# Performance work log

Measured on AMD Instinct MI355X. Metric: run time of the kernel, lower is better.

## Reference

```python
import jax, jax.numpy as jnp
import numpy as np

B, L, DM, H = 2, 2048, 512, 8
D = DM // H
FACTOR = 5
NUM_K = int(FACTOR * np.ceil(np.log(L)))  # 40
NUM_Q = NUM_K  # q_len == k_len here
EPS = 1e-5


def setup_inputs() -> dict:
    key = jax.random.key(0)
    ks = jax.random.split(key, 12)
    s = DM ** -0.5
    return {
        "q": jax.random.normal(ks[0], (B, L, DM), jnp.float32),
        "k": jax.random.normal(ks[1], (B, L, DM), jnp.float32),
        "v": jax.random.normal(ks[2], (B, L, DM), jnp.float32),
        "Wq": jax.random.normal(ks[3], (DM, DM), jnp.float32) * s,
        "bq": jnp.zeros((DM,), jnp.float32),
        "Wk": jax.random.normal(ks[4], (DM, DM), jnp.float32) * s,
        "bk": jnp.zeros((DM,), jnp.float32),
        "Wv": jax.random.normal(ks[5], (DM, DM), jnp.float32) * s,
        "bv": jnp.zeros((DM,), jnp.float32),
        "gamma": jnp.ones((DM,), jnp.float32),
        "beta": jnp.zeros((DM,), jnp.float32),
        "random_index": jax.random.randint(ks[6], (L, NUM_K), 0, L, jnp.int32),
    }


def _heads(x):
    # [B, L, DM] -> [B, H, L, D]
    return x.reshape(B, L, H, D).transpose(0, 2, 1, 3)


def reference(q, k, v, Wq, bq, Wk, bk, Wv, bv, gamma, beta, random_index):
    qp = _heads(q @ Wq + bq)
    kp = _heads(k @ Wk + bk)
    vp = _heads(v @ Wv + bv)

    # ProbSparse: sample NUM_K keys per query position (shared over batch/head)
    k_samp = kp[:, :, random_index, :]                      # [B,H,L,NUM_K,D]
    pre = jnp.einsum('bhid,bhijd->bhij', qp, k_samp)        # [B,H,L,NUM_K]
    measure = pre.max(-1) - pre.sum(-1) / L                 # sparsity measure [B,H,L]
    _, q_idx = jax.lax.top_k(measure, NUM_Q)                # [B,H,NUM_Q]

    q_sel = jnp.take_along_axis(qp, q_idx[..., None], axis=2)   # [B,H,NUM_Q,D]
    attn = jnp.einsum('bhid,bhjd->bhij', q_sel, kp) * D ** -0.5 # [B,H,NUM_Q,L]
    attn = jax.nn.softmax(attn, axis=-1)                    # dropout = identity (eval)
    out_sel = jnp.einsum('bhij,bhjd->bhid', attn, vp)       # [B,H,NUM_Q,D]

    # use_mask=False path: context is the mean of v over keys
    v_mean = vp.mean(axis=2)                                # [B,H,D]
    context = jnp.broadcast_to(v_mean[:, :, None, :], (B, H, L, D))
    bi = jnp.arange(B)[:, None, None]
    hi = jnp.arange(H)[None, :, None]
    out = context.at[bi, hi, q_idx].set(out_sel)            # scatter selected rows

    out = out.transpose(0, 2, 1, 3).reshape(B, L, DM)
    y = out + q
    mu = y.mean(-1, keepdims=True)
    var = y.var(-1, keepdims=True)
    yn = (y - mu) / jnp.sqrt(var + EPS) * gamma + beta
    return (yn, attn)
```

## Files before the change

### kernel.cpp

```cpp
#include <hip/hip_runtime.h>
#include <math.h>

#define BB 2
#define LL 2048
#define DMM 512
#define HH 8
#define DD 64
#define NUMK 40
#define NUMQ 40
#define LNEPS 1e-5f
#define LSEG 128
#define NLS 16

typedef unsigned short ushort_t;
typedef __attribute__((ext_vector_type(8))) short bf16x8;
typedef __attribute__((ext_vector_type(4))) float f32x4;

__device__ inline ushort_t f2bf(float x) {
    union { float f; unsigned int u; } v; v.f = x;
    unsigned int r = v.u + 0x7fffu + ((v.u >> 16) & 1u);
    return (ushort_t)(r >> 16);
}
__device__ inline float bf2f(ushort_t h) {
    union { unsigned int u; float f; } v; v.u = ((unsigned int)h) << 16;
    return v.f;
}

__global__ __launch_bounds__(256) void convert_all_kernel(
    const float* __restrict__ q, const float* __restrict__ k, const float* __restrict__ v,
    const float* __restrict__ Wq, const float* __restrict__ Wk, const float* __restrict__ Wv,
    ushort_t* __restrict__ Xh, ushort_t* __restrict__ Xl,
    ushort_t* __restrict__ Wht, ushort_t* __restrict__ Wlt) {
    __shared__ float tile[64][65];
    const int bx = blockIdx.x;
    const int t = threadIdx.x;
    if (bx < 3072) {
        const int y = bx >> 10, x = bx & 1023;
        const size_t plane = (size_t)BB * LL * DMM;
        const float* X = (y == 0) ? q : (y == 1) ? k : v;
        ushort_t* xh = Xh + plane * y;
        ushort_t* xl = Xl + plane * y;
        const size_t base = ((size_t)x * 256 + t) * 8;
        float4 a = *(const float4*)(X + base);
        float4 b = *(const float4*)(X + base + 4);
        float xs[8] = {a.x, a.y, a.z, a.w, b.x, b.y, b.z, b.w};
        unsigned int hp[4], lp[4];
#pragma unroll
        for (int j = 0; j < 4; ++j) {
            ushort_t h0 = f2bf(xs[2 * j]),     h1 = f2bf(xs[2 * j + 1]);
            ushort_t l0 = f2bf(xs[2 * j] - bf2f(h0));
            ushort_t l1 = f2bf(xs[2 * j + 1] - bf2f(h1));
            hp[j] = (unsigned int)h0 | ((unsigned int)h1 << 16);
            lp[j] = (unsigned int)l0 | ((unsigned int)l1 << 16);
        }
        *(uint4*)(xh + base) = make_uint4(hp[0], hp[1], hp[2], hp[3]);
        *(uint4*)(xl + base) = make_uint4(lp[0], lp[1], lp[2], lp[3]);
    } else {
        const int idx = bx - 3072;
        const int z = idx >> 6, rem = idx & 63;
        const size_t plane = (size_t)DMM * DMM;
        const float* W = (z == 0) ? Wq : (z == 1) ? Wk : Wv;
        ushort_t* wht = Wht + plane * z;
        ushort_t* wlt = Wlt + plane * z;
        const int n0 = (rem & 7) * 64, k0 = (rem >> 3) * 64;
        const int d = t & 63, g = t >> 6;
        for (int rr = g; rr < 64; rr += 4)
            tile[rr][d] = W[(size_t)(k0 + rr) * DMM + n0 + d];
        __syncthreads();
        for (int cc = g; cc < 64; cc += 4) {
            float x = tile[d][cc];
            ushort_t hi = f2bf(x);
            ushort_t lo = f2bf(x - bf2f(hi));
            wht[(size_t)(n0 + cc) * DMM + k0 + d] = hi;
            wlt[(size_t)(n0 + cc) * DMM + k0 + d] = lo;
        }
    }
}

__device__ inline void stage_one(const ushort_t* __restrict__ g, ushort_t* lbuf,
                                 int r0, int lane, int k0) {
    const int r = r0 + (lane >> 3);
    const int c = (lane & 7) ^ (r & 7);
    const ushort_t* gp = g + (size_t)r * DMM + k0 + c * 8;
    __builtin_amdgcn_global_load_lds(
        (const __attribute__((address_space(1))) unsigned int*)gp,
        (__attribute__((address_space(3))) unsigned int*)(lbuf + (size_t)r0 * 64),
        16, 0, 0);
}
__device__ inline bf16x8 frag_ld(const ushort_t* buf, int row, int c) {
    const int idx = row * 8 + (c ^ (row & 7));
    return *(const bf16x8*)(buf + idx * 8);
}

__global__ __launch_bounds__(256, 2) void proj_mfma_kernel(
    const ushort_t* __restrict__ Xh, const ushort_t* __restrict__ Xl,
    const ushort_t* __restrict__ Wht, const ushort_t* __restrict__ Wlt,
    const float* __restrict__ bq, const float* __restrict__ bk, const float* __restrict__ bv,
    float* __restrict__ Oq, float* __restrict__ Ok, float* __restrict__ Ov) {
    const int orig = blockIdx.x;
    const int c = (orig & 7) * 48 + (orig >> 3);
    const int jb = c & 3, mb = (c >> 2) & 31, z = c >> 7;

    const size_t xplane = (size_t)BB * LL * DMM;
    const size_t wplane = (size_t)DMM * DMM;
    const ushort_t* ah_g = Xh + xplane * z;
    const ushort_t* al_g = Xl + xplane * z;
    const ushort_t* bh_g = Wht + wplane * z;
    const ushort_t* bl_g = Wlt + wplane * z;
    const float* bias = (z == 0) ? bq : (z == 1) ? bk : bv;
    float* Out = (z == 0) ? Oq : (z == 1) ? Ok : Ov;

    __shared__ __align__(16) ushort_t bufAh[128 * 64];
    __shared__ __align__(16) ushort_t bufAl[128 * 64];
    __shared__ __align__(16) ushort_t bufBh[128 * 64];
    __shared__ __align__(16) ushort_t bufBl[128 * 64];

    const int t = threadIdx.x;
    const int lane = t & 63, w = t >> 6;
    const int wm = (w & 1) * 64, wn = (w >> 1) * 64;
    const int m0 = mb * 128, j0 = jb * 128;

    const ushort_t* A_h = ah_g + (size_t)m0 * DMM;
    const ushort_t* A_l = al_g + (size_t)m0 * DMM;
    const ushort_t* B_h = bh_g + (size_t)j0 * DMM;
    const ushort_t* B_l = bl_g + (size_t)j0 * DMM;

    f32x4 acc[4][4];
#pragma unroll
    for (int i = 0; i < 4; ++i)
#pragma unroll
        for (int j = 0; j < 4; ++j) acc[i][j] = (f32x4){0.f, 0.f, 0.f, 0.f};

    for (int ch = 0; ch < 8; ++ch) {
        const int k0 = ch * 64;
#pragma unroll
        for (int i = 0; i < 4; ++i) {
            const int r0 = (w * 4 + i) * 8;
            stage_one(A_h, bufAh, r0, lane, k0);
            stage_one(A_l, bufAl, r0, lane, k0);
            stage_one(B_h, bufBh, r0, lane, k0);
            stage_one(B_l, bufBl, r0, lane, k0);
        }
        __syncthreads();
#pragma unroll
        for (int ks = 0; ks < 2; ++ks) {
            const int cc = ks * 4 + (lane >> 4);
            bf16x8 fah[4], fal[4];
#pragma unroll
            for (int tm = 0; tm < 4; ++tm) {
                const int row = wm + tm * 16 + (lane & 15);
                fah[tm] = frag_ld(bufAh, row, cc);
                fal[tm] = frag_ld(bufAl, row, cc);
            }
#pragma unroll
            for (int tn = 0; tn < 4; ++tn) {
                const int rowb = wn + tn * 16 + (lane & 15);
                const bf16x8 fbh = frag_ld(bufBh, rowb, cc);
                const bf16x8 fbl = frag_ld(bufBl, rowb, cc);
#pragma unroll
                for (int tm = 0; tm < 4; ++tm) {
                    acc[tm][tn] = __builtin_amdgcn_mfma_f32_16x16x32_bf16(fah[tm], fbh, acc[tm][tn], 0, 0, 0);
                    acc[tm][tn] = __builtin_amdgcn_mfma_f32_16x16x32_bf16(fal[tm], fbh, acc[tm][tn], 0, 0, 0);
                    acc[tm][tn] = __builtin_amdgcn_mfma_f32_16x16x32_bf16(fah[tm], fbl, acc[tm][tn], 0, 0, 0);
                }
            }
        }
        __syncthreads();
    }

#pragma unroll
    for (int tn = 0; tn < 4; ++tn) {
        const int gn = j0 + wn + tn * 16 + (lane & 15);
        const float bvv = bias[gn];
        const int h = gn >> 6, d = gn & 63;
#pragma unroll
        for (int tm = 0; tm < 4; ++tm) {
#pragma unroll
            for (int reg = 0; reg < 4; ++reg) {
                const int gm = m0 + wm + tm * 16 + (lane >> 4) * 4 + reg;
                const int b = gm >> 11, l = gm & (LL - 1);
                Out[(((size_t)(b * HH + h)) * LL + l) * DD + d] = acc[tm][tn][reg] + bvv;
            }
        }
    }
}

__global__ __launch_bounds__(256) void measure_vmean_kernel(
    const float* __restrict__ qp2, const float* __restrict__ kp2,
    const float* __restrict__ vp2, const int* __restrict__ rnd,
    float* __restrict__ measure, float* __restrict__ partial) {
    __shared__ float pv[256];
    const int bx = blockIdx.x;
    const int t = threadIdx.x;
    if (bx < 2048) {
        const int c = (bx & 7) * 256 + (bx >> 3);
        const int lane = t & 63;
        const int wv = t >> 6;
        const int g = lane >> 4;
        const int dq = (lane & 15) * 4;
        const int bh = c >> 7;
        const int i = (c & 127) * 16 + wv * 4 + g;
        const float4 qv = *(const float4*)(qp2 + ((size_t)bh * LL + i) * DD + dq);
        const float* kbase = kp2 + (size_t)bh * LL * DD;
        const int* rp = rnd + i * NUMK;
        float mx = -INFINITY, sm = 0.f;
#pragma unroll 8
        for (int j = 0; j < NUMK; ++j) {
            const int row = rp[j];
            const float4 kv = *(const float4*)(kbase + (size_t)row * DD + dq);
            float p = kv.x * qv.x;
            p = fmaf(kv.y, qv.y, p); p = fmaf(kv.z, qv.z, p); p = fmaf(kv.w, qv.w, p);
            p += __shfl_xor(p, 1, 64);
            p += __shfl_xor(p, 2, 64);
            p += __shfl_xor(p, 4, 64);
            p += __shfl_xor(p, 8, 64);
            mx = fmaxf(mx, p);
            sm += p;
        }
        if ((lane & 15) == 0) measure[(size_t)bh * LL + i] = mx - sm * (1.0f / LL);
    } else {
        const int idx = bx - 2048;
        const int chunk = idx & 31;
        const int bh = idx >> 5;
        const int d = t & 63, g = t >> 6;
        const int l0 = chunk * 64;
        float acc = 0.f;
        for (int l = l0 + g; l < l0 + 64; l += 4)
            acc += vp2[((size_t)bh * LL + l) * DD + d];
        pv[t] = acc;
        __syncthreads();
        if (t < 64)
            partial[(size_t)idx * 64 + t] = pv[t] + pv[64 + t] + pv[128 + t] + pv[192 + t];
    }
}

__global__ __launch_bounds__(256) void topk_kernel(const float* __restrict__ measure,
                                                   const float* __restrict__ partial,
                                                   int* __restrict__ q_idx,
                                                   int* __restrict__ sel_pos,
                                                   float* __restrict__ v_mean) {
    __shared__ unsigned int keys[LL];
    __shared__ int hist[256];
    __shared__ unsigned int prefix_sh;
    __shared__ int need_sh;
    __shared__ unsigned int cval[256];
    __shared__ int cidx[256];
    __shared__ int cnt;
    const int t = threadIdx.x;
    const int lane = t & 63;
    const int bh = blockIdx.x;
    for (int i = t; i < LL; i += 256) {
        const float f = measure[(size_t)bh * LL + i];
        unsigned int u = __float_as_uint(f);
        keys[i] = (u & 0x80000000u) ? ~u : (u | 0x80000000u);
        sel_pos[(size_t)bh * LL + i] = -1;
    }
    if (t < 64) {
        float s = 0.f;
        for (int c = 0; c < 32; ++c)
            s += partial[((size_t)bh * 32 + c) * 64 + t];
        v_mean[bh * 64 + t] = s * (1.0f / LL);
    }
    if (t == 0) { prefix_sh = 0u; need_sh = NUMQ; cnt = 0; }
    __syncthreads();

    for (int round = 0; round < 4; ++round) {
        const int shift = 24 - round * 8;
        hist[t] = 0;
        __syncthreads();
        const unsigned int pref = prefix_sh;
        if (round == 0) {
            for (int i = t; i < LL; i += 256) {
                const int b = (int)(keys[i] >> 24);
                unsigned long long rem = ~0ull;
                while (rem) {
                    const int leader = __ffsll((long long)rem) - 1;
                    const int b0 = __shfl(b, leader, 64);
                    const unsigned long long same = __ballot(b == b0) & rem;
                    if (lane == leader) atomicAdd(&hist[b0], (int)__popcll(same));
                    rem &= ~same;
                }
            }
        } else {
            const unsigned int mask = 0xFFFFFFFFu << (shift + 8);
            for (int i = t; i < LL; i += 256) {
                const unsigned int key = keys[i];
                if ((key & mask) == pref)
                    atomicAdd(&hist[(key >> shift) & 0xFF], 1);
            }
        }
        __syncthreads();
        if (t < 64) {
            const int b0 = hist[4 * t + 0], b1 = hist[4 * t + 1];
            const int b2 = hist[4 * t + 2], b3 = hist[4 * t + 3];
            const int loc = b0 + b1 + b2 + b3;
            int suf = loc;
#pragma unroll
            for (int off = 1; off < 64; off <<= 1) {
                const int other = __shfl_down(suf, off, 64);
                if (lane + off < 64) suf += other;
            }
            const int need = need_sh;
            int s[5];
            s[0] = suf;
            s[1] = suf - b0;
            s[2] = suf - b0 - b1;
            s[3] = suf - b0 - b1 - b2;
            s[4] = suf - loc;
#pragma unroll
            for (int kk = 0; kk < 4; ++kk) {
                if (s[kk] >= need && s[kk + 1] < need) {
                    need_sh = need - s[kk + 1];
                    prefix_sh = pref | ((unsigned int)(4 * t + kk) << shift);
                }
            }
        }
        __syncthreads();
    }
    const unsigned int K40 = prefix_sh;

    for (int i = t; i < LL; i += 256) {
        if (keys[i] >= K40) {
            int p = atomicAdd(&cnt, 1);
            if (p < 256) { cval[p] = keys[i]; cidx[p] = i; }
        }
    }
    __syncthreads();
    int M = cnt; if (M > 256) M = 256;
    for (int i = t; i < M; i += 256) {
        const unsigned int ki = cval[i];
        const int ii = cidx[i];
        int r = 0;
        for (int j = 0; j < M; ++j) {
            const unsigned int kj = cval[j];
            r += (kj > ki || (kj == ki && cidx[j] < ii)) ? 1 : 0;
        }
        if (r < NUMQ) {
            q_idx[bh * NUMQ + r] = ii;
            sel_pos[(size_t)bh * LL + ii] = r;
        }
    }
}

__global__ __launch_bounds__(256) void attn_part_kernel(
    const float* __restrict__ qp2, const float* __restrict__ kp2,
    const float* __restrict__ vp2, const int* __restrict__ q_idx,
    float* __restrict__ attn_out, float* __restrict__ part_m,
    float* __restrict__ part_s, float* __restrict__ part_pv) {
    __shared__ __align__(16) float Qs[NUMQ][68];
    __shared__ __align__(16) float Ks[LSEG * 64];
    __shared__ __align__(16) float Vs[LSEG * 64];
    __shared__ __align__(16) float Ss[NUMQ][136];
    const int t = threadIdx.x;
    const int lane = t & 63, w = t >> 6;
    const int bh = blockIdx.x;
    const int ls = blockIdx.y;
    const int l0 = ls * LSEG;

    for (int idx = t; idx < NUMQ * 16; idx += 256) {
        const int r = idx >> 4, c4 = idx & 15;
        const int qi = q_idx[bh * NUMQ + r];
        float4 v = *(const float4*)(qp2 + ((size_t)bh * LL + qi) * DD + c4 * 4);
        Qs[r][c4 * 4 + 0] = v.x * 0.125f;
        Qs[r][c4 * 4 + 1] = v.y * 0.125f;
        Qs[r][c4 * 4 + 2] = v.z * 0.125f;
        Qs[r][c4 * 4 + 3] = v.w * 0.125f;
    }

    const float* kseg = kp2 + ((size_t)bh * LL + l0) * DD;
    const float* vseg = vp2 + ((size_t)bh * LL + l0) * DD;
#pragma unroll
    for (int i = 0; i < 8; ++i) {
        const int r0 = (w * 8 + i) * 4;
        const int r = r0 + (lane >> 4);
        const int cg = (lane & 15) ^ (r & 15);
        __builtin_amdgcn_global_load_lds(
            (const __attribute__((address_space(1))) unsigned int*)(kseg + (size_t)r * DD + cg * 4),
            (__attribute__((address_space(3))) unsigned int*)(Ks + r0 * 64), 16, 0, 0);
        __builtin_amdgcn_global_load_lds(
            (const __attribute__((address_space(1))) unsigned int*)(vseg + (size_t)r * DD + cg * 4),
            (__attribute__((address_space(3))) unsigned int*)(Vs + r0 * 64), 16, 0, 0);
    }
    __syncthreads();

    const int qt = t >> 5;
    const int jt = t & 31;
    float acc[5][4];
#pragma unroll
    for (int i = 0; i < 5; ++i)
#pragma unroll
        for (int jj = 0; jj < 4; ++jj) acc[i][jj] = 0.f;

    for (int c4 = 0; c4 < 16; ++c4) {
        float4 q4[5];
#pragma unroll
        for (int i = 0; i < 5; ++i)
            q4[i] = *(const float4*)&Qs[qt + 8 * i][c4 * 4];
#pragma unroll
        for (int jj = 0; jj < 4; ++jj) {
            const int r = jt + 32 * jj;
            const float4 k4 = *(const float4*)&Ks[r * 64 + ((c4 ^ (r & 15)) * 4)];
#pragma unroll
            for (int i = 0; i < 5; ++i) {
                acc[i][jj] = fmaf(q4[i].x, k4.x, acc[i][jj]);
                acc[i][jj] = fmaf(q4[i].y, k4.y, acc[i][jj]);
                acc[i][jj] = fmaf(q4[i].z, k4.z, acc[i][jj]);
                acc[i][jj] = fmaf(q4[i].w, k4.w, acc[i][jj]);
            }
        }
    }

#pragma unroll
    for (int i = 0; i < 5; ++i) {
        const int r = qt + 8 * i;
        float m = fmaxf(fmaxf(acc[i][0], acc[i][1]), fmaxf(acc[i][2], acc[i][3]));
        m = fmaxf(m, __shfl_xor(m, 16, 64));
        m = fmaxf(m, __shfl_xor(m, 8, 64));
        m = fmaxf(m, __shfl_xor(m, 4, 64));
        m = fmaxf(m, __shfl_xor(m, 2, 64));
        m = fmaxf(m, __shfl_xor(m, 1, 64));
        float p0 = __expf(acc[i][0] - m), p1 = __expf(acc[i][1] - m);
        float p2 = __expf(acc[i][2] - m), p3 = __expf(acc[i][3] - m);
        Ss[r][jt]      = p0;
        Ss[r][jt + 32] = p1;
        Ss[r][jt + 64] = p2;
        Ss[r][jt + 96] = p3;
        float s = p0 + p1 + p2 + p3;
        s += __shfl_xor(s, 16, 64);
        s += __shfl_xor(s, 8, 64);
        s += __shfl_xor(s, 4, 64);
        s += __shfl_xor(s, 2, 64);
        s += __shfl_xor(s, 1, 64);
        if (jt == 0) {
            const int row = bh * NUMQ + r;
            part_m[row * NLS + ls] = m;
            part_s[row * NLS + ls] = s;
        }
    }
    __syncthreads();

    for (int idx = t; idx < NUMQ * 32; idx += 256) {
        const int r = idx >> 5, c4 = idx & 31;
        const float4 v = *(const float4*)&Ss[r][c4 * 4];
        *(float4*)(attn_out + (size_t)(bh * NUMQ + r) * LL + l0 + c4 * 4) = v;
    }

    const int dt = t & 31;
    float o[5][2];
#pragma unroll
    for (int i = 0; i < 5; ++i) { o[i][0] = 0.f; o[i][1] = 0.f; }
#pragma unroll 2
    for (int j0_ = 0; j0_ < LSEG; j0_ += 4) {
        float4 p4[5];
#pragma unroll
        for (int i = 0; i < 5; ++i)
            p4[i] = *(const float4*)&Ss[qt + 8 * i][j0_];
#pragma unroll
        for (int jj = 0; jj < 4; ++jj) {
            const int j = j0_ + jj;
            const int pg = (dt >> 1) ^ (j & 15);
            const float* vr = &Vs[j * 64 + pg * 4 + (dt & 1) * 2];
            const float v0 = vr[0], v1 = vr[1];
#pragma unroll
            for (int i = 0; i < 5; ++i) {
                const float p = ((const float*)&p4[i])[jj];
                o[i][0] = fmaf(p, v0, o[i][0]);
                o[i][1] = fmaf(p, v1, o[i][1]);
            }
        }
    }
#pragma unroll
    for (int i = 0; i < 5; ++i) {
        const int row = bh * NUMQ + qt + 8 * i;
        float* pp = part_pv + ((size_t)row * NLS + ls) * DD + dt * 2;
        pp[0] = o[i][0];
        pp[1] = o[i][1];
    }
}

__global__ __launch_bounds__(512) void final_all_kernel(
    const float* __restrict__ q_in, const int* __restrict__ sel_pos,
    const float* __restrict__ part_m, const float* __restrict__ part_s,
    const float* __restrict__ part_pv, const float* __restrict__ v_mean,
    const float* __restrict__ gamma, const float* __restrict__ beta,
    float* __restrict__ attn_out, float* __restrict__ yout) {
    __shared__ float wred[8];
    const int bx = blockIdx.x;
    const int j = threadIdx.x;
    if (bx >= BB * LL) {
        const int row = bx - BB * LL;
        float M = -INFINITY;
#pragma unroll
        for (int i = 0; i < NLS; ++i) M = fmaxf(M, part_m[row * NLS + i]);
        float T = 0.f;
#pragma unroll
        for (int i = 0; i < NLS; ++i)
            T += part_s[row * NLS + i] * __expf(part_m[row * NLS + i] - M);
        const float inv = 1.0f / T;
        const int s0 = j >> 5;
        const float g = __expf(part_m[row * NLS + s0] - M) * inv;
        float* arow = attn_out + (size_t)row * LL;
        float4 v = *(const float4*)&arow[4 * j];
        v.x *= g; v.y *= g; v.z *= g; v.w *= g;
        *(float4*)&arow[4 * j] = v;
        return;
    }
    const int lane = j & 63, wv = j >> 6;
    const int tok = bx;
    const int b = tok >> 11;
    const int l = tok & (LL - 1);
    const int h = wv, d = lane;
    const int bh = b * HH + h;
    const int p = sel_pos[(size_t)bh * LL + l];
    float val;
    if (p >= 0) {
        const int row = bh * NUMQ + p;
        float M = -INFINITY;
#pragma unroll
        for (int i = 0; i < NLS; ++i) M = fmaxf(M, part_m[row * NLS + i]);
        float T = 0.f, s = 0.f;
#pragma unroll
        for (int i = 0; i < NLS; ++i) {
            const float e = __expf(part_m[row * NLS + i] - M);
            T += part_s[row * NLS + i] * e;
            s += part_pv[((size_t)row * NLS + i) * DD + d] * e;
        }
        val = s * (1.0f / T);
    } else {
        val = v_mean[bh * DD + d];
    }
    float y = val + q_in[(size_t)tok * DMM + j];
    float s = y;
#pragma unroll
    for (int off = 32; off > 0; off >>= 1) s += __shfl_xor(s, off, 64);
    if (lane == 0) wred[wv] = s;
    __syncthreads();
    float tot = 0.f;
#pragma unroll
    for (int u = 0; u < 8; ++u) tot += wred[u];
    float mu = tot * (1.0f / DMM);
    __syncthreads();
    float dv = y - mu;
    float s2 = dv * dv;
#pragma unroll
    for (int off = 32; off > 0; off >>= 1) s2 += __shfl_xor(s2, off, 64);
    if (lane == 0) wred[wv] = s2;
    __syncthreads();
    float tot2 = 0.f;
#pragma unroll
    for (int u = 0; u < 8; ++u) tot2 += wred[u];
    float var = tot2 * (1.0f / DMM);
    float yn = dv * rsqrtf(var + LNEPS) * gamma[j] + beta[j];
    yout[(size_t)tok * DMM + j] = yn;
}

extern "C" void kernel_launch(void* const* d_in, const int* in_sizes, int n_in,
                              void* d_out, int out_size, void* d_ws, size_t ws_size,
                              hipStream_t stream) {
    const float* q     = (const float*)d_in[0];
    const float* k     = (const float*)d_in[1];
    const float* v     = (const float*)d_in[2];
    const float* Wq    = (const float*)d_in[3];
    const float* bq    = (const float*)d_in[4];
    const float* Wk    = (const float*)d_in[5];
    const float* bk    = (const float*)d_in[6];
    const float* Wv    = (const float*)d_in[7];
    const float* bv    = (const float*)d_in[8];
    const float* gamma = (const float*)d_in[9];
    const float* beta  = (const float*)d_in[10];
    const int*   rnd   = (const int*)d_in[11];

    float* ws = (float*)d_ws;
    const size_t proj_sz = (size_t)BB * HH * LL * DD;
    float* qp2     = ws;
    float* kp2     = qp2 + proj_sz;
    float* vp2     = kp2 + proj_sz;
    float* measure = vp2 + proj_sz;
    float* out_sel = measure + (size_t)BB * HH * LL;
    float* v_mean  = out_sel + (size_t)BB * HH * NUMQ * DD;
    float* partial = v_mean + (size_t)BB * HH * DD;
    float* part_m  = partial + (size_t)BB * HH * 32 * 64;
    float* part_s  = part_m + (size_t)BB * HH * NUMQ * NLS;
    float* part_pv = part_s + (size_t)BB * HH * NUMQ * NLS;
    int*   q_idx   = (int*)(part_pv + (size_t)BB * HH * NUMQ * NLS * DD);
    int*   sel_pos = q_idx + BB * HH * NUMQ;
    ushort_t* Xh  = (ushort_t*)(sel_pos + BB * HH * LL);
    ushort_t* Xl  = Xh + 3 * proj_sz;
    ushort_t* Wht = Xl + 3 * proj_sz;
    ushort_t* Wlt = Wht + 3 * (size_t)DMM * DMM;

    float* yn_out   = (float*)d_out;
    float* attn_out = yn_out + (size_t)BB * LL * DMM;

    convert_all_kernel<<<3072 + 192, 256, 0, stream>>>(q, k, v, Wq, Wk, Wv, Xh, Xl, Wht, Wlt);
    proj_mfma_kernel<<<dim3(3 * (BB * LL / 128) * (DMM / 128), 1, 1), 256, 0, stream>>>(
        Xh, Xl, Wht, Wlt, bq, bk, bv, qp2, kp2, vp2);
    measure_vmean_kernel<<<2048 + 512, 256, 0, stream>>>(qp2, kp2, vp2, rnd, measure, partial);
    topk_kernel<<<BB * HH, 256, 0, stream>>>(measure, partial, q_idx, sel_pos, v_mean);
    attn_part_kernel<<<dim3(BB * HH, NLS), 256, 0, stream>>>(
        qp2, kp2, vp2, q_idx, attn_out, part_m, part_s, part_pv);
    final_all_kernel<<<BB * LL + BB * HH * NUMQ, 512, 0, stream>>>(
        q, sel_pos, part_m, part_s, part_pv, v_mean, gamma, beta, attn_out, yn_out);
}
```

Baseline: 176.5 us.

## Fuse fp32-to-bf16 split of activations into projection GEMM with register prefetch

```diff
diff --git a/kernel.cpp b/kernel.cpp
--- a/kernel.cpp
+++ b/kernel.cpp
@@ -26,59 +26,33 @@
     return v.f;
 }
 
-__global__ __launch_bounds__(256) void convert_all_kernel(
-    const float* __restrict__ q, const float* __restrict__ k, const float* __restrict__ v,
+__global__ __launch_bounds__(256) void convert_w_kernel(
     const float* __restrict__ Wq, const float* __restrict__ Wk, const float* __restrict__ Wv,
-    ushort_t* __restrict__ Xh, ushort_t* __restrict__ Xl,
     ushort_t* __restrict__ Wht, ushort_t* __restrict__ Wlt) {
     __shared__ float tile[64][65];
-    const int bx = blockIdx.x;
+    const int idx = blockIdx.x;
+    const int z = idx >> 6, rem = idx & 63;
+    const size_t plane = (size_t)DMM * DMM;
+    const float* W = (z == 0) ? Wq : (z == 1) ? Wk : Wv;
+    ushort_t* wht = Wht + plane * z;
+    ushort_t* wlt = Wlt + plane * z;
+    const int n0 = (rem & 7) * 64, k0 = (rem >> 3) * 64;
     const int t = threadIdx.x;
-    if (bx < 3072) {
-        const int y = bx >> 10, x = bx & 1023;
-        const size_t plane = (size_t)BB * LL * DMM;
-        const float* X = (y == 0) ? q : (y == 1) ? k : v;
-        ushort_t* xh = Xh + plane * y;
-        ushort_t* xl = Xl + plane * y;
-        const size_t base = ((size_t)x * 256 + t) * 8;
-        float4 a = *(const float4*)(X + base);
-        float4 b = *(const float4*)(X + base + 4);
-        float xs[8] = {a.x, a.y, a.z, a.w, b.x, b.y, b.z, b.w};
-        unsigned int hp[4], lp[4];
-#pragma unroll
-        for (int j = 0; j < 4; ++j) {
-            ushort_t h0 = f2bf(xs[2 * j]),     h1 = f2bf(xs[2 * j + 1]);
-            ushort_t l0 = f2bf(xs[2 * j] - bf2f(h0));
-            ushort_t l1 = f2bf(xs[2 * j + 1] - bf2f(h1));
-            hp[j] = (unsigned int)h0 | ((unsigned int)h1 << 16);
-            lp[j] = (unsigned int)l0 | ((unsigned int)l1 << 16);
-        }
-        *(uint4*)(xh + base) = make_uint4(hp[0], hp[1], hp[2], hp[3]);
-        *(uint4*)(xl + base) = make_uint4(lp[0], lp[1], lp[2], lp[3]);
-    } else {
-        const int idx = bx - 3072;
-        const int z = idx >> 6, rem = idx & 63;
-        const size_t plane = (size_t)DMM * DMM;
-        const float* W = (z == 0) ? Wq : (z == 1) ? Wk : Wv;
-        ushort_t* wht = Wht + plane * z;
-        ushort_t* wlt = Wlt + plane * z;
-        const int n0 = (rem & 7) * 64, k0 = (rem >> 3) * 64;
-        const int d = t & 63, g = t >> 6;
-        for (int rr = g; rr < 64; rr += 4)
-            tile[rr][d] = W[(size_t)(k0 + rr) * DMM + n0 + d];
-        __syncthreads();
-        for (int cc = g; cc < 64; cc += 4) {
-            float x = tile[d][cc];
-            ushort_t hi = f2bf(x);
-            ushort_t lo = f2bf(x - bf2f(hi));
-            wht[(size_t)(n0 + cc) * DMM + k0 + d] = hi;
-            wlt[(size_t)(n0 + cc) * DMM + k0 + d] = lo;
-        }
-    }
-}
-
-__device__ inline void stage_one(const ushort_t* __restrict__ g, ushort_t* lbuf,
-                                 int r0, int lane, int k0) {
+    const int d = t & 63, g = t >> 6;
+    for (int rr = g; rr < 64; rr += 4)
+        tile[rr][d] = W[(size_t)(k0 + rr) * DMM + n0 + d];
+    __syncthreads();
+    for (int cc = g; cc < 64; cc += 4) {
+        float x = tile[d][cc];
+        ushort_t hi = f2bf(x);
+        ushort_t lo = f2bf(x - bf2f(hi));
+        wht[(size_t)(n0 + cc) * DMM + k0 + d] = hi;
+        wlt[(size_t)(n0 + cc) * DMM + k0 + d] = lo;
+    }
+}
+
+__device__ inline void stage_oneB(const ushort_t* __restrict__ g, ushort_t* lbuf,
+                                  int r0, int lane, int k0) {
     const int r = r0 + (lane >> 3);
     const int c = (lane & 7) ^ (r & 7);
     const ushort_t* gp = g + (size_t)r * DMM + k0 + c * 8;
@@ -93,7 +67,7 @@
 }
 
 __global__ __launch_bounds__(256, 2) void proj_mfma_kernel(
-    const ushort_t* __restrict__ Xh, const ushort_t* __restrict__ Xl,
+    const float* __restrict__ Xq, const float* __restrict__ Xk, const float* __restrict__ Xv,
     const ushort_t* __restrict__ Wht, const ushort_t* __restrict__ Wlt,
     const float* __restrict__ bq, const float* __restrict__ bk, const float* __restrict__ bv,
     float* __restrict__ Oq, float* __restrict__ Ok, float* __restrict__ Ov) {
@@ -101,10 +75,8 @@
     const int c = (orig & 7) * 48 + (orig >> 3);
     const int jb = c & 3, mb = (c >> 2) & 31, z = c >> 7;
 
-    const size_t xplane = (size_t)BB * LL * DMM;
     const size_t wplane = (size_t)DMM * DMM;
-    const ushort_t* ah_g = Xh + xplane * z;
-    const ushort_t* al_g = Xl + xplane * z;
+    const float* X32 = (z == 0) ? Xq : (z == 1) ? Xk : Xv;
     const ushort_t* bh_g = Wht + wplane * z;
     const ushort_t* bl_g = Wlt + wplane * z;
     const float* bias = (z == 0) ? bq : (z == 1) ? bk : bv;
@@ -120,28 +92,64 @@
     const int wm = (w & 1) * 64, wn = (w >> 1) * 64;
     const int m0 = mb * 128, j0 = jb * 128;
 
-    const ushort_t* A_h = ah_g + (size_t)m0 * DMM;
-    const ushort_t* A_l = al_g + (size_t)m0 * DMM;
+    const float* A32 = X32 + (size_t)m0 * DMM;
     const ushort_t* B_h = bh_g + (size_t)j0 * DMM;
     const ushort_t* B_l = bl_g + (size_t)j0 * DMM;
 
-    f32x4 acc[4][4];
-#pragma unroll
-    for (int i = 0; i < 4; ++i)
-#pragma unroll
-        for (int j = 0; j < 4; ++j) acc[i][j] = (f32x4){0.f, 0.f, 0.f, 0.f};
-
-    for (int ch = 0; ch < 8; ++ch) {
-        const int k0 = ch * 64;
+    const int ag = t & 7;
+    const int ar = t >> 3;
+
+    float4 a0[4], a1[4];
+    auto load_a = [&](int k0v) {
+#pragma unroll
+        for (int kk = 0; kk < 4; ++kk) {
+            const float* src = A32 + (size_t)(ar + 32 * kk) * DMM + k0v + ag * 8;
+            a0[kk] = *(const float4*)src;
+            a1[kk] = *(const float4*)(src + 4);
+        }
+    };
+    auto write_a = [&]() {
+#pragma unroll
+        for (int kk = 0; kk < 4; ++kk) {
+            const int r = ar + 32 * kk;
+            const float xs[8] = {a0[kk].x, a0[kk].y, a0[kk].z, a0[kk].w,
+                                 a1[kk].x, a1[kk].y, a1[kk].z, a1[kk].w};
+            unsigned int hp[4], lp[4];
+#pragma unroll
+            for (int j = 0; j < 4; ++j) {
+                const ushort_t h0 = f2bf(xs[2 * j]),     h1 = f2bf(xs[2 * j + 1]);
+                const ushort_t l0 = f2bf(xs[2 * j] - bf2f(h0));
+                const ushort_t l1 = f2bf(xs[2 * j + 1] - bf2f(h1));
+                hp[j] = (unsigned int)h0 | ((unsigned int)h1 << 16);
+                lp[j] = (unsigned int)l0 | ((unsigned int)l1 << 16);
+            }
+            const int slot = r * 8 + (ag ^ (r & 7));
+            *(uint4*)(bufAh + slot * 8) = make_uint4(hp[0], hp[1], hp[2], hp[3]);
+            *(uint4*)(bufAl + slot * 8) = make_uint4(lp[0], lp[1], lp[2], lp[3]);
+        }
+    };
+    auto stage_b = [&](int k0v) {
 #pragma unroll
         for (int i = 0; i < 4; ++i) {
             const int r0 = (w * 4 + i) * 8;
-            stage_one(A_h, bufAh, r0, lane, k0);
-            stage_one(A_l, bufAl, r0, lane, k0);
-            stage_one(B_h, bufBh, r0, lane, k0);
-            stage_one(B_l, bufBl, r0, lane, k0);
-        }
+            stage_oneB(B_h, bufBh, r0, lane, k0v);
+            stage_oneB(B_l, bufBl, r0, lane, k0v);
+        }
+    };
+
+    f32x4 acc[4][4];
+#pragma unroll
+    for (int i = 0; i < 4; ++i)
+#pragma unroll
+        for (int j = 0; j < 4; ++j) acc[i][j] = (f32x4){0.f, 0.f, 0.f, 0.f};
+
+    load_a(0);
+    write_a();
+    stage_b(0);
+
+    for (int ch = 0; ch < 8; ++ch) {
         __syncthreads();
+        if (ch < 7) load_a((ch + 1) * 64);
 #pragma unroll
         for (int ks = 0; ks < 2; ++ks) {
             const int cc = ks * 4 + (lane >> 4);
@@ -166,6 +174,7 @@
             }
         }
         __syncthreads();
+        if (ch < 7) { write_a(); stage_b((ch + 1) * 64); }
     }
 
 #pragma unroll
@@ -584,17 +593,15 @@
     float* part_pv = part_s + (size_t)BB * HH * NUMQ * NLS;
     int*   q_idx   = (int*)(part_pv + (size_t)BB * HH * NUMQ * NLS * DD);
     int*   sel_pos = q_idx + BB * HH * NUMQ;
-    ushort_t* Xh  = (ushort_t*)(sel_pos + BB * HH * LL);
-    ushort_t* Xl  = Xh + 3 * proj_sz;
-    ushort_t* Wht = Xl + 3 * proj_sz;
+    ushort_t* Wht = (ushort_t*)(sel_pos + BB * HH * LL);
     ushort_t* Wlt = Wht + 3 * (size_t)DMM * DMM;
 
     float* yn_out   = (float*)d_out;
     float* attn_out = yn_out + (size_t)BB * LL * DMM;
 
-    convert_all_kernel<<<3072 + 192, 256, 0, stream>>>(q, k, v, Wq, Wk, Wv, Xh, Xl, Wht, Wlt);
+    convert_w_kernel<<<192, 256, 0, stream>>>(Wq, Wk, Wv, Wht, Wlt);
     proj_mfma_kernel<<<dim3(3 * (BB * LL / 128) * (DMM / 128), 1, 1), 256, 0, stream>>>(
-        Xh, Xl, Wht, Wlt, bq, bk, bv, qp2, kp2, vp2);
+        q, k, v, Wht, Wlt, bq, bk, bv, qp2, kp2, vp2);
     measure_vmean_kernel<<<2048 + 512, 256, 0, stream>>>(qp2, kp2, vp2, rnd, measure, partial);
     topk_kernel<<<BB * HH, 256, 0, stream>>>(measure, partial, q_idx, sel_pos, v_mean);
     attn_part_kernel<<<dim3(BB * HH, NLS), 256, 0, stream>>>(
```

New measurement: 180.8 us. +2.4%, slower.
